# Performance work log

Measured on AMD Instinct MI355X. Metric: run time of the kernel, lower is better.

Reference implementation:

```python
import jax, jax.numpy as jnp
import numpy as np

EMBED_DIM = 1024
NUM_HEADS = 16
HEAD_DIM = EMBED_DIM // NUM_HEADS


def setup_inputs() -> dict:
    key = jax.random.key(0)
    k_x, k_qw, k_qb, k_ow, k_ob = jax.random.split(key, 5)
    B, T, C = 4, 2048, EMBED_DIM
    s = 1.0 / np.sqrt(C)
    return {
        "x": jax.random.normal(k_x, (B, T, C), dtype=jnp.float32),
        # torch nn.Linear weights: [out_features, in_features]
        "qkv_w": jax.random.uniform(k_qw, (3 * C, C), jnp.float32, -s, s),
        "qkv_b": jax.random.uniform(k_qb, (3 * C,), jnp.float32, -s, s),
        "out_w": jax.random.uniform(k_ow, (C, C), jnp.float32, -s, s),
        "out_b": jax.random.uniform(k_ob, (C,), jnp.float32, -s, s),
    }


def reference(x, qkv_w, qkv_b, out_w, out_b):
    B, T, C = x.shape
    H, D = NUM_HEADS, HEAD_DIM
    qkv = x @ qkv_w.T + qkv_b                      # [B,T,3C]
    qkv = qkv.reshape(B, T, 3, H, D).transpose(2, 0, 3, 1, 4)  # [3,B,H,T,D]
    Q, K, V = qkv[0], qkv[1], qkv[2]
    scores = jnp.einsum("bhtd,bhsd->bhts", Q, K) / np.sqrt(D).astype(np.float32)
    causal = jnp.triu(jnp.ones((T, T), dtype=bool), k=1)        # mask future
    scores = jnp.where(causal, -jnp.inf, scores)
    attn_weights = jax.nn.softmax(scores, axis=-1)              # [B,H,T,T]
    out = jnp.einsum("bhts,bhsd->bhtd", attn_weights, V)
    out = out.transpose(0, 2, 1, 3).reshape(B, T, C)
    return out @ out_w.T + out_b, attn_weights
```

## Files before the change

kernel.cpp:

```cpp
#include <hip/hip_runtime.h>
#include <cstdint>
#include <cstddef>

#define Bq  4
#define Tq  2048
#define Cq  1024
#define Hq  16
#define Dq  64
#define BTq 8192
#define C3q 3072

using bf16x8 = __attribute__((ext_vector_type(8))) short;
using f32x4  = __attribute__((ext_vector_type(4))) float;
using us4    = __attribute__((ext_vector_type(4))) unsigned short;

__device__ __forceinline__ unsigned short f2bf(float f) {
  unsigned u = __builtin_bit_cast(unsigned, f);
  return (unsigned short)((u + 0x7fffu + ((u >> 16) & 1u)) >> 16);
}
__device__ __forceinline__ float bf2f(unsigned short h) {
  return __builtin_bit_cast(float, (unsigned)h << 16);
}

__device__ __forceinline__ void gload_lds16(const void* g, void* l) {
  __builtin_amdgcn_global_load_lds(
      (const __attribute__((address_space(1))) void*)g,
      (__attribute__((address_space(3))) void*)l, 16, 0, 0);
}

__global__ __launch_bounds__(256) void cvt_kernel(const float* __restrict__ src,
                                                  unsigned short* __restrict__ dst, int n4) {
  int i = blockIdx.x * 256 + threadIdx.x;
  int stride = gridDim.x * 256;
  for (; i < n4; i += stride) {
    float4 v = reinterpret_cast<const float4*>(src)[i];
    us4 o = { f2bf(v.x), f2bf(v.y), f2bf(v.z), f2bf(v.w) };
    reinterpret_cast<us4*>(dst)[i] = o;
  }
}

template<int EPI>
__global__ __launch_bounds__(256) void gemm128(
    const unsigned short* __restrict__ A, const unsigned short* __restrict__ Bw,
    const float* __restrict__ bias,
    unsigned short* __restrict__ Qb, unsigned short* __restrict__ Kb,
    unsigned short* __restrict__ Vtb, float* __restrict__ Cout,
    int M, int N, int K)
{
  __shared__ unsigned short As[128][32];
  __shared__ unsigned short Bs[128][32];
  const int n0 = blockIdx.x * 128, m0 = blockIdx.y * 128;
  const int tid = threadIdx.x;
  const int w = tid >> 6, l = tid & 63, r = l & 15, g = l >> 4;
  const int wm = w >> 1, wn = w & 1;
  const int ldRow = tid >> 2, ldCol = (tid & 3) * 8;
  f32x4 acc[4][4] = {};

  const unsigned short* Ar0 = A  + (size_t)(m0 +      ldRow) * K + ldCol;
  const unsigned short* Ar1 = A  + (size_t)(m0 + 64 + ldRow) * K + ldCol;
  const unsigned short* Br0 = Bw + (size_t)(n0 +      ldRow) * K + ldCol;
  const unsigned short* Br1 = Bw + (size_t)(n0 + 64 + ldRow) * K + ldCol;
  char* Ab0 = (char*)&As[0][0]        + w * 1024;
  char* Ab1 = (char*)&As[0][0] + 4096 + w * 1024;
  char* Bb0 = (char*)&Bs[0][0]        + w * 1024;
  char* Bb1 = (char*)&Bs[0][0] + 4096 + w * 1024;

  for (int k0 = 0; k0 < K; k0 += 32) {
    __syncthreads();
    gload_lds16(Ar0 + k0, Ab0);
    gload_lds16(Ar1 + k0, Ab1);
    gload_lds16(Br0 + k0, Bb0);
    gload_lds16(Br1 + k0, Bb1);
    __syncthreads();
    bf16x8 a[4], b[4];
    #pragma unroll
    for (int i = 0; i < 4; ++i) a[i] = *(const bf16x8*)&As[wm*64 + i*16 + r][g*8];
    #pragma unroll
    for (int j = 0; j < 4; ++j) b[j] = *(const bf16x8*)&Bs[wn*64 + j*16 + r][g*8];
    #pragma unroll
    for (int i = 0; i < 4; ++i)
      #pragma unroll
      for (int j = 0; j < 4; ++j)
        acc[i][j] = __builtin_amdgcn_mfma_f32_16x16x32_bf16(a[i], b[j], acc[i][j], 0, 0, 0);
  }

  if (EPI == 0) {
    const int which = n0 >> 10;
    #pragma unroll
    for (int i = 0; i < 4; ++i)
      #pragma unroll
      for (int j = 0; j < 4; ++j) {
        int gc  = n0 + wn*64 + j*16 + r;
        int gr0 = m0 + wm*64 + i*16 + 4*g;
        float bv = bias[gc];
        int hd = gc & 1023;
        int h = hd >> 6, d = hd & 63;
        if (which == 2) {
          int b = gr0 >> 11, t0 = gr0 & 2047;
          int bh = b*Hq + h;
          us4 pk = { f2bf(acc[i][j][0] + bv), f2bf(acc[i][j][1] + bv),
                     f2bf(acc[i][j][2] + bv), f2bf(acc[i][j][3] + bv) };
          *(us4*)&Vtb[(size_t)(bh*Dq + d)*Tq + t0] = pk;
        } else {
          unsigned short* dst = which ? Kb : Qb;
          #pragma unroll
          for (int jj = 0; jj < 4; ++jj) {
            int gr = gr0 + jj;
            int b = gr >> 11, t = gr & 2047;
            int bh = b*Hq + h;
            dst[(size_t)(bh*Tq + t)*Dq + d] = f2bf(acc[i][j][jj] + bv);
          }
        }
      }
  } else {
    #pragma unroll
    for (int i = 0; i < 4; ++i)
      #pragma unroll
      for (int j = 0; j < 4; ++j) {
        int gc = n0 + wn*64 + j*16 + r;
        float bv = bias[gc];
        #pragma unroll
        for (int jj = 0; jj < 4; ++jj) {
          int gr = m0 + wm*64 + i*16 + 4*g + jj;
          Cout[(size_t)gr * N + gc] = acc[i][j][jj] + bv;
        }
      }
  }
}

#define PROWB 4224

__global__ __launch_bounds__(256) void attn_kernel(
    const unsigned short* __restrict__ Qb, const unsigned short* __restrict__ Kb,
    const unsigned short* __restrict__ Vtb,
    float* __restrict__ attn, unsigned short* __restrict__ ctxb)
{
  __shared__ __align__(16) unsigned short P[16][2112];
  __shared__ float red[4][32];
  __shared__ float invl_s[32];

  const int p  = blockIdx.x;
  const int bh = blockIdx.y;
  const int tid = threadIdx.x, w = tid >> 6, l = tid & 63, r = l & 15, g = l >> 4;
  const int qbA = p * 16, qbB = (127 - p) * 16;
  const int NA = (qbA + 16 + 31) >> 5;
  const int NB = (qbB + 16 + 31) >> 5;
  const int LAc = NA * 32, LBc = NB * 32;

  const unsigned short* Qp = Qb  + (size_t)bh * Tq * Dq;
  const unsigned short* Kp = Kb  + (size_t)bh * Tq * Dq;
  const unsigned short* Vp = Vtb + (size_t)bh * Dq * Tq;
  char* Pmut = (char*)&P[0][0];

  bf16x8 aqA0 = *(const bf16x8*)&Qp[(size_t)(qbA + r)*Dq      + g*8];
  bf16x8 aqA1 = *(const bf16x8*)&Qp[(size_t)(qbA + r)*Dq + 32 + g*8];
  bf16x8 aqB0 = *(const bf16x8*)&Qp[(size_t)(qbB + r)*Dq      + g*8];
  bf16x8 aqB1 = *(const bf16x8*)&Qp[(size_t)(qbB + r)*Dq + 32 + g*8];

  float lsumA[4] = {0.f,0.f,0.f,0.f}, lsumB[4] = {0.f,0.f,0.f,0.f};

#define CHUNK(k0_, qb_, cb_, q0_, q1_, lsum_)                                       \
  {                                                                                 \
    const int k0c = (k0_);                                                          \
    f32x4 z = {0.f,0.f,0.f,0.f};                                                    \
    bf16x8 bk00 = *(const bf16x8*)&Kp[(size_t)(k0c + r)*Dq      + g*8];             \
    bf16x8 bk01 = *(const bf16x8*)&Kp[(size_t)(k0c + r)*Dq + 32 + g*8];             \
    bf16x8 bk10 = *(const bf16x8*)&Kp[(size_t)(k0c + 16 + r)*Dq      + g*8];        \
    bf16x8 bk11 = *(const bf16x8*)&Kp[(size_t)(k0c + 16 + r)*Dq + 32 + g*8];        \
    __builtin_amdgcn_s_setprio(1);                                                  \
    f32x4 s0 = __builtin_amdgcn_mfma_f32_16x16x32_bf16(q0_, bk00, z, 0, 0, 0);      \
    s0 = __builtin_amdgcn_mfma_f32_16x16x32_bf16(q1_, bk01, s0, 0, 0, 0);           \
    f32x4 s1 = __builtin_amdgcn_mfma_f32_16x16x32_bf16(q0_, bk10, z, 0, 0, 0);      \
    s1 = __builtin_amdgcn_mfma_f32_16x16x32_bf16(q1_, bk11, s1, 0, 0, 0);           \
    __builtin_amdgcn_s_setprio(0);                                                  \
    _Pragma("unroll")                                                               \
    for (int jj = 0; jj < 4; ++jj) {                                                \
      int q = (qb_) + 4*g + jj;                                                     \
      float p0 = (k0c + r      <= q) ? __expf(s0[jj]*0.125f) : 0.f;                 \
      float p1 = (k0c + 16 + r <= q) ? __expf(s1[jj]*0.125f) : 0.f;                 \
      lsum_[jj] += p0 + p1;                                                         \
      int row = 4*g + jj, xm = (row & 7) << 4;                                      \
      *(unsigned short*)(Pmut + row*PROWB + ((((cb_) + r)*2)      ^ xm)) = f2bf(p0);\
      *(unsigned short*)(Pmut + row*PROWB + ((((cb_) + 16 + r)*2) ^ xm)) = f2bf(p1);\
    }                                                                               \
  }

  for (int cj = w; cj < NA; cj += 4)
    CHUNK(cj*32, qbA, cj*32, aqA0, aqA1, lsumA);
  for (int cj = (w - NA) & 3; cj < NB; cj += 4)
    CHUNK(cj*32, qbB, LAc + cj*32, aqB0, aqB1, lsumB);

  #pragma unroll
  for (int jj = 0; jj < 4; ++jj) {
    float sa = lsumA[jj], sb = lsumB[jj];
    #pragma unroll
    for (int off = 1; off < 16; off <<= 1) {
      sa += __shfl_xor(sa, off, 64);
      sb += __shfl_xor(sb, off, 64);
    }
    if (r == 0) { red[w][4*g + jj] = sa; red[w][16 + 4*g + jj] = sb; }
  }
  __syncthreads();
  if (tid < 32) {
    float s = red[0][tid] + red[1][tid] + red[2][tid] + red[3][tid];
    invl_s[tid] = 1.f / s;
  }
  __syncthreads();

  const int row16 = tid >> 4, seg = (tid & 15) * 8;
  const int xm16 = (row16 & 7) << 4;
  const char* Prow = Pmut + row16 * PROWB;
  {
    float inv = invl_s[row16];
    size_t ob = ((size_t)bh*Tq + qbA + row16) * Tq;
    for (int cb = seg; cb < Tq; cb += 128) {
      f32x4 v0 = {0.f,0.f,0.f,0.f}, v1 = {0.f,0.f,0.f,0.f};
      if (cb < LAc) {
        bf16x8 pv = *(const bf16x8*)(Prow + ((cb*2) ^ xm16));
        v0[0]=bf2f((unsigned short)pv[0])*inv; v0[1]=bf2f((unsigned short)pv[1])*inv;
        v0[2]=bf2f((unsigned short)pv[2])*inv; v0[3]=bf2f((unsigned short)pv[3])*inv;
        v1[0]=bf2f((unsigned short)pv[4])*inv; v1[1]=bf2f((unsigned short)pv[5])*inv;
        v1[2]=bf2f((unsigned short)pv[6])*inv; v1[3]=bf2f((unsigned short)pv[7])*inv;
      }
      __builtin_nontemporal_store(v0, (f32x4*)&attn[ob + cb]);
      __builtin_nontemporal_store(v1, (f32x4*)&attn[ob + cb + 4]);
    }
  }
  {
    float inv = invl_s[16 + row16];
    size_t ob = ((size_t)bh*Tq + qbB + row16) * Tq;
    for (int cb = seg; cb < Tq; cb += 128) {
      f32x4 v0 = {0.f,0.f,0.f,0.f}, v1 = {0.f,0.f,0.f,0.f};
      if (cb < LBc) {
        bf16x8 pv = *(const bf16x8*)(Prow + (((LAc + cb)*2) ^ xm16));
        v0[0]=bf2f((unsigned short)pv[0])*inv; v0[1]=bf2f((unsigned short)pv[1])*inv;
        v0[2]=bf2f((unsigned short)pv[2])*inv; v0[3]=bf2f((unsigned short)pv[3])*inv;
        v1[0]=bf2f((unsigned short)pv[4])*inv; v1[1]=bf2f((unsigned short)pv[5])*inv;
        v1[2]=bf2f((unsigned short)pv[6])*inv; v1[3]=bf2f((unsigned short)pv[7])*inv;
      }
      __builtin_nontemporal_store(v0, (f32x4*)&attn[ob + cb]);
      __builtin_nontemporal_store(v1, (f32x4*)&attn[ob + cb + 4]);
    }
  }

  f32x4 coA = {0.f,0.f,0.f,0.f}, coB = {0.f,0.f,0.f,0.f};
  const char* Pr = Pmut + r * PROWB;
  const int xr = (r & 7) << 4;
  const unsigned short* Vrow = &Vp[(size_t)(w*16 + r) * Tq];
  for (int cj = 0; cj < NA; ++cj) {
    int k0 = cj*32;
    bf16x8 pa = *(const bf16x8*)(Pr + (((k0 + g*8)*2) ^ xr));
    bf16x8 bv = *(const bf16x8*)&Vrow[k0 + g*8];
    coA = __builtin_amdgcn_mfma_f32_16x16x32_bf16(pa, bv, coA, 0, 0, 0);
  }
  for (int cj = 0; cj < NB; ++cj) {
    int k0 = cj*32;
    bf16x8 pa = *(const bf16x8*)(Pr + (((LAc + k0 + g*8)*2) ^ xr));
    bf16x8 bv = *(const bf16x8*)&Vrow[k0 + g*8];
    coB = __builtin_amdgcn_mfma_f32_16x16x32_bf16(pa, bv, coB, 0, 0, 0);
  }

  const int b = bh >> 4, h = bh & 15;
  #pragma unroll
  for (int jj = 0; jj < 4; ++jj) {
    int tA = qbA + 4*g + jj;
    ctxb[(size_t)(b*Tq + tA)*Cq + h*Dq + w*16 + r] = f2bf(coA[jj] * invl_s[4*g + jj]);
    int tB = qbB + 4*g + jj;
    ctxb[(size_t)(b*Tq + tB)*Cq + h*Dq + w*16 + r] = f2bf(coB[jj] * invl_s[16 + 4*g + jj]);
  }
#undef CHUNK
}

extern "C" void kernel_launch(void* const* d_in, const int* in_sizes, int n_in,
                              void* d_out, int out_size, void* d_ws, size_t ws_size,
                              hipStream_t stream) {
  const float* x     = (const float*)d_in[0];
  const float* qkv_w = (const float*)d_in[1];
  const float* qkv_b = (const float*)d_in[2];
  const float* out_w = (const float*)d_in[3];
  const float* out_b = (const float*)d_in[4];
  float* out  = (float*)d_out;
  float* attn = out + (size_t)BTq * Cq;

  char* ws = (char*)d_ws;
  unsigned short* xb    = (unsigned short*)(ws);
  unsigned short* wqkvb = (unsigned short*)(ws + (16u << 20));
  unsigned short* woutb = (unsigned short*)(ws + (22u << 20));
  unsigned short* Qb    = (unsigned short*)(ws + (24u << 20));
  unsigned short* Kb    = (unsigned short*)(ws + (40u << 20));
  unsigned short* Vtb   = (unsigned short*)(ws + (56u << 20));
  unsigned short* ctxb  = (unsigned short*)(ws + (72u << 20));

  cvt_kernel<<<2048, 256, 0, stream>>>(x,     xb,    (BTq * Cq) / 4);
  cvt_kernel<<<1024, 256, 0, stream>>>(qkv_w, wqkvb, (C3q * Cq) / 4);
  cvt_kernel<<<512,  256, 0, stream>>>(out_w, woutb, (Cq * Cq) / 4);

  dim3 g1(C3q / 128, BTq / 128);
  gemm128<0><<<g1, 256, 0, stream>>>(xb, wqkvb, qkv_b, Qb, Kb, Vtb, nullptr, BTq, C3q, Cq);

  dim3 g2(64, Bq * Hq);
  attn_kernel<<<g2, 256, 0, stream>>>(Qb, Kb, Vtb, attn, ctxb);

  dim3 g3(Cq / 128, BTq / 128);
  gemm128<1><<<g3, 256, 0, stream>>>(ctxb, woutb, out_b, nullptr, nullptr, nullptr, out, BTq, Cq, Cq);
}
```

Before: 554.5 us.

## Double attention block to 512 threads with prefetched K chunks and split PV reduction

```diff
diff --git a/kernel.cpp b/kernel.cpp
--- a/kernel.cpp
+++ b/kernel.cpp
@@ -129,15 +129,17 @@
 }
 
 #define PROWB 4224
-
-__global__ __launch_bounds__(256) void attn_kernel(
+#define XMASK(row_) ((((row_) & 7) << 4) ^ ((((row_) >> 2) & 3) << 5))
+
+__global__ __launch_bounds__(512, 4) void attn_kernel(
     const unsigned short* __restrict__ Qb, const unsigned short* __restrict__ Kb,
     const unsigned short* __restrict__ Vtb,
     float* __restrict__ attn, unsigned short* __restrict__ ctxb)
 {
   __shared__ __align__(16) unsigned short P[16][2112];
-  __shared__ float red[4][32];
+  __shared__ float red[8][32];
   __shared__ float invl_s[32];
+  __shared__ f32x4 Cred[4][2][64];
 
   const int p  = blockIdx.x;
   const int bh = blockIdx.y;
@@ -159,36 +161,52 @@
 
   float lsumA[4] = {0.f,0.f,0.f,0.f}, lsumB[4] = {0.f,0.f,0.f,0.f};
 
-#define CHUNK(k0_, qb_, cb_, q0_, q1_, lsum_)                                       \
+#define LOADK(ci_, D00, D01, D10, D11)                                              \
   {                                                                                 \
-    const int k0c = (k0_);                                                          \
-    f32x4 z = {0.f,0.f,0.f,0.f};                                                    \
-    bf16x8 bk00 = *(const bf16x8*)&Kp[(size_t)(k0c + r)*Dq      + g*8];             \
-    bf16x8 bk01 = *(const bf16x8*)&Kp[(size_t)(k0c + r)*Dq + 32 + g*8];             \
-    bf16x8 bk10 = *(const bf16x8*)&Kp[(size_t)(k0c + 16 + r)*Dq      + g*8];        \
-    bf16x8 bk11 = *(const bf16x8*)&Kp[(size_t)(k0c + 16 + r)*Dq + 32 + g*8];        \
-    __builtin_amdgcn_s_setprio(1);                                                  \
-    f32x4 s0 = __builtin_amdgcn_mfma_f32_16x16x32_bf16(q0_, bk00, z, 0, 0, 0);      \
-    s0 = __builtin_amdgcn_mfma_f32_16x16x32_bf16(q1_, bk01, s0, 0, 0, 0);           \
-    f32x4 s1 = __builtin_amdgcn_mfma_f32_16x16x32_bf16(q0_, bk10, z, 0, 0, 0);      \
-    s1 = __builtin_amdgcn_mfma_f32_16x16x32_bf16(q1_, bk11, s1, 0, 0, 0);           \
-    __builtin_amdgcn_s_setprio(0);                                                  \
-    _Pragma("unroll")                                                               \
-    for (int jj = 0; jj < 4; ++jj) {                                                \
-      int q = (qb_) + 4*g + jj;                                                     \
-      float p0 = (k0c + r      <= q) ? __expf(s0[jj]*0.125f) : 0.f;                 \
-      float p1 = (k0c + 16 + r <= q) ? __expf(s1[jj]*0.125f) : 0.f;                 \
-      lsum_[jj] += p0 + p1;                                                         \
-      int row = 4*g + jj, xm = (row & 7) << 4;                                      \
-      *(unsigned short*)(Pmut + row*PROWB + ((((cb_) + r)*2)      ^ xm)) = f2bf(p0);\
-      *(unsigned short*)(Pmut + row*PROWB + ((((cb_) + 16 + r)*2) ^ xm)) = f2bf(p1);\
-    }                                                                               \
-  }
-
-  for (int cj = w; cj < NA; cj += 4)
-    CHUNK(cj*32, qbA, cj*32, aqA0, aqA1, lsumA);
-  for (int cj = (w - NA) & 3; cj < NB; cj += 4)
-    CHUNK(cj*32, qbB, LAc + cj*32, aqB0, aqB1, lsumB);
+    int cj_ = ((ci_) < NA) ? (ci_) : (ci_) - NA;                                    \
+    int k0c_ = cj_ * 32;                                                            \
+    D00 = *(const bf16x8*)&Kp[(size_t)(k0c_ + r)*Dq      + g*8];                    \
+    D01 = *(const bf16x8*)&Kp[(size_t)(k0c_ + r)*Dq + 32 + g*8];                    \
+    D10 = *(const bf16x8*)&Kp[(size_t)(k0c_ + 16 + r)*Dq      + g*8];               \
+    D11 = *(const bf16x8*)&Kp[(size_t)(k0c_ + 16 + r)*Dq + 32 + g*8];               \
+  }
+
+  {
+    bf16x8 k00, k01, k10, k11, n00, n01, n10, n11;
+    int ci = w;
+    if (ci < 65) LOADK(ci, k00, k01, k10, k11);
+    for (; ci < 65; ci += 8) {
+      if (ci + 8 < 65) LOADK(ci + 8, n00, n01, n10, n11);
+      const bool isA = ci < NA;
+      const int cj  = isA ? ci : ci - NA;
+      const int k0c = cj * 32;
+      const int qb_ = isA ? qbA : qbB;
+      const int cb_ = isA ? k0c : LAc + k0c;
+      bf16x8 q0_ = isA ? aqA0 : aqB0;
+      bf16x8 q1_ = isA ? aqA1 : aqB1;
+      f32x4 z = {0.f,0.f,0.f,0.f};
+      __builtin_amdgcn_s_setprio(1);
+      f32x4 s0 = __builtin_amdgcn_mfma_f32_16x16x32_bf16(q0_, k00, z, 0, 0, 0);
+      s0 = __builtin_amdgcn_mfma_f32_16x16x32_bf16(q1_, k01, s0, 0, 0, 0);
+      f32x4 s1 = __builtin_amdgcn_mfma_f32_16x16x32_bf16(q0_, k10, z, 0, 0, 0);
+      s1 = __builtin_amdgcn_mfma_f32_16x16x32_bf16(q1_, k11, s1, 0, 0, 0);
+      __builtin_amdgcn_s_setprio(0);
+      float tch[4];
+      #pragma unroll
+      for (int jj = 0; jj < 4; ++jj) {
+        int q = qb_ + 4*g + jj;
+        float p0 = (k0c + r      <= q) ? __expf(s0[jj]*0.125f) : 0.f;
+        float p1 = (k0c + 16 + r <= q) ? __expf(s1[jj]*0.125f) : 0.f;
+        tch[jj] = p0 + p1;
+        int row = 4*g + jj, xm = XMASK(row);
+        *(unsigned short*)(Pmut + row*PROWB + (((cb_ + r)*2)      ^ xm)) = f2bf(p0);
+        *(unsigned short*)(Pmut + row*PROWB + (((cb_ + 16 + r)*2) ^ xm)) = f2bf(p1);
+      }
+      if (isA) { lsumA[0]+=tch[0]; lsumA[1]+=tch[1]; lsumA[2]+=tch[2]; lsumA[3]+=tch[3]; }
+      else     { lsumB[0]+=tch[0]; lsumB[1]+=tch[1]; lsumB[2]+=tch[2]; lsumB[3]+=tch[3]; }
+      k00 = n00; k01 = n01; k10 = n10; k11 = n11;
+    }
+  }
 
   #pragma unroll
   for (int jj = 0; jj < 4; ++jj) {
@@ -202,21 +220,27 @@
   }
   __syncthreads();
   if (tid < 32) {
-    float s = red[0][tid] + red[1][tid] + red[2][tid] + red[3][tid];
+    float s = 0.f;
+    #pragma unroll
+    for (int ww = 0; ww < 8; ++ww) s += red[ww][tid];
     invl_s[tid] = 1.f / s;
   }
   __syncthreads();
 
-  const int row16 = tid >> 4, seg = (tid & 15) * 8;
-  const int xm16 = (row16 & 7) << 4;
-  const char* Prow = Pmut + row16 * PROWB;
   {
-    float inv = invl_s[row16];
-    size_t ob = ((size_t)bh*Tq + qbA + row16) * Tq;
+    const int s16   = tid >> 8;
+    const int row16 = (tid >> 4) & 15;
+    const int seg   = (tid & 15) * 8;
+    const int xm16  = XMASK(row16);
+    const char* Prow = Pmut + row16 * PROWB;
+    const int Lc    = s16 ? LBc : LAc;
+    const int cbase = s16 ? LAc : 0;
+    float inv = invl_s[s16*16 + row16];
+    size_t ob = ((size_t)bh*Tq + (s16 ? qbB : qbA) + row16) * Tq;
     for (int cb = seg; cb < Tq; cb += 128) {
       f32x4 v0 = {0.f,0.f,0.f,0.f}, v1 = {0.f,0.f,0.f,0.f};
-      if (cb < LAc) {
-        bf16x8 pv = *(const bf16x8*)(Prow + ((cb*2) ^ xm16));
+      if (cb < Lc) {
+        bf16x8 pv = *(const bf16x8*)(Prow + (((cbase + cb)*2) ^ xm16));
         v0[0]=bf2f((unsigned short)pv[0])*inv; v0[1]=bf2f((unsigned short)pv[1])*inv;
         v0[2]=bf2f((unsigned short)pv[2])*inv; v0[3]=bf2f((unsigned short)pv[3])*inv;
         v1[0]=bf2f((unsigned short)pv[4])*inv; v1[1]=bf2f((unsigned short)pv[5])*inv;
@@ -226,49 +250,51 @@
       __builtin_nontemporal_store(v1, (f32x4*)&attn[ob + cb + 4]);
     }
   }
+
+  f32x4 coA = {0.f,0.f,0.f,0.f}, coB = {0.f,0.f,0.f,0.f};
   {
-    float inv = invl_s[16 + row16];
-    size_t ob = ((size_t)bh*Tq + qbB + row16) * Tq;
-    for (int cb = seg; cb < Tq; cb += 128) {
-      f32x4 v0 = {0.f,0.f,0.f,0.f}, v1 = {0.f,0.f,0.f,0.f};
-      if (cb < LBc) {
-        bf16x8 pv = *(const bf16x8*)(Prow + (((LAc + cb)*2) ^ xm16));
-        v0[0]=bf2f((unsigned short)pv[0])*inv; v0[1]=bf2f((unsigned short)pv[1])*inv;
-        v0[2]=bf2f((unsigned short)pv[2])*inv; v0[3]=bf2f((unsigned short)pv[3])*inv;
-        v1[0]=bf2f((unsigned short)pv[4])*inv; v1[1]=bf2f((unsigned short)pv[5])*inv;
-        v1[2]=bf2f((unsigned short)pv[6])*inv; v1[3]=bf2f((unsigned short)pv[7])*inv;
-      }
-      __builtin_nontemporal_store(v0, (f32x4*)&attn[ob + cb]);
-      __builtin_nontemporal_store(v1, (f32x4*)&attn[ob + cb + 4]);
-    }
-  }
-
-  f32x4 coA = {0.f,0.f,0.f,0.f}, coB = {0.f,0.f,0.f,0.f};
-  const char* Pr = Pmut + r * PROWB;
-  const int xr = (r & 7) << 4;
-  const unsigned short* Vrow = &Vp[(size_t)(w*16 + r) * Tq];
-  for (int cj = 0; cj < NA; ++cj) {
-    int k0 = cj*32;
-    bf16x8 pa = *(const bf16x8*)(Pr + (((k0 + g*8)*2) ^ xr));
-    bf16x8 bv = *(const bf16x8*)&Vrow[k0 + g*8];
-    coA = __builtin_amdgcn_mfma_f32_16x16x32_bf16(pa, bv, coA, 0, 0, 0);
-  }
-  for (int cj = 0; cj < NB; ++cj) {
-    int k0 = cj*32;
-    bf16x8 pa = *(const bf16x8*)(Pr + (((LAc + k0 + g*8)*2) ^ xr));
-    bf16x8 bv = *(const bf16x8*)&Vrow[k0 + g*8];
-    coB = __builtin_amdgcn_mfma_f32_16x16x32_bf16(pa, bv, coB, 0, 0, 0);
-  }
-
-  const int b = bh >> 4, h = bh & 15;
-  #pragma unroll
-  for (int jj = 0; jj < 4; ++jj) {
-    int tA = qbA + 4*g + jj;
-    ctxb[(size_t)(b*Tq + tA)*Cq + h*Dq + w*16 + r] = f2bf(coA[jj] * invl_s[4*g + jj]);
-    int tB = qbB + 4*g + jj;
-    ctxb[(size_t)(b*Tq + tB)*Cq + h*Dq + w*16 + r] = f2bf(coB[jj] * invl_s[16 + 4*g + jj]);
-  }
-#undef CHUNK
+    const int dblk = w & 3, par = w >> 2;
+    const char* Pr = Pmut + r * PROWB;
+    const int xr = XMASK(r);
+    const unsigned short* Vrow = &Vp[(size_t)(dblk*16 + r) * Tq];
+    bf16x8 pa, bv, pan, bvn;
+    int ci = par;
+    {
+      int cj = (ci < NA) ? ci : ci - NA;
+      int cb = (ci < NA) ? ci*32 : LAc + cj*32;
+      pa = *(const bf16x8*)(Pr + (((cb + g*8)*2) ^ xr));
+      bv = *(const bf16x8*)&Vrow[cj*32 + g*8];
+    }
+    for (; ci < 65; ci += 2) {
+      if (ci + 2 < 65) {
+        int cn = ci + 2;
+        int cj = (cn < NA) ? cn : cn - NA;
+        int cb = (cn < NA) ? cn*32 : LAc + cj*32;
+        pan = *(const bf16x8*)(Pr + (((cb + g*8)*2) ^ xr));
+        bvn = *(const bf16x8*)&Vrow[cj*32 + g*8];
+      }
+      if (ci < NA) coA = __builtin_amdgcn_mfma_f32_16x16x32_bf16(pa, bv, coA, 0, 0, 0);
+      else         coB = __builtin_amdgcn_mfma_f32_16x16x32_bf16(pa, bv, coB, 0, 0, 0);
+      pa = pan; bv = bvn;
+    }
+    if (par == 1) { Cred[dblk][0][l] = coA; Cred[dblk][1][l] = coB; }
+  }
+  __syncthreads();
+  if ((w >> 2) == 0) {
+    const int dblk = w & 3;
+    f32x4 cA = Cred[dblk][0][l], cB = Cred[dblk][1][l];
+    coA[0]+=cA[0]; coA[1]+=cA[1]; coA[2]+=cA[2]; coA[3]+=cA[3];
+    coB[0]+=cB[0]; coB[1]+=cB[1]; coB[2]+=cB[2]; coB[3]+=cB[3];
+    const int b = bh >> 4, h = bh & 15;
+    #pragma unroll
+    for (int jj = 0; jj < 4; ++jj) {
+      int tA = qbA + 4*g + jj;
+      ctxb[(size_t)(b*Tq + tA)*Cq + h*Dq + dblk*16 + r] = f2bf(coA[jj] * invl_s[4*g + jj]);
+      int tB = qbB + 4*g + jj;
+      ctxb[(size_t)(b*Tq + tB)*Cq + h*Dq + dblk*16 + r] = f2bf(coB[jj] * invl_s[16 + 4*g + jj]);
+    }
+  }
+#undef LOADK
 }
 
 extern "C" void kernel_launch(void* const* d_in, const int* in_sizes, int n_in,
@@ -299,7 +325,7 @@
   gemm128<0><<<g1, 256, 0, stream>>>(xb, wqkvb, qkv_b, Qb, Kb, Vtb, nullptr, BTq, C3q, Cq);
 
   dim3 g2(64, Bq * Hq);
-  attn_kernel<<<g2, 256, 0, stream>>>(Qb, Kb, Vtb, attn, ctxb);
+  attn_kernel<<<g2, 512, 0, stream>>>(Qb, Kb, Vtb, attn, ctxb);
 
   dim3 g3(Cq / 128, BTq / 128);
   gemm128<1><<<g3, 256, 0, stream>>>(ctxb, woutb, out_b, nullptr, nullptr, nullptr, out, BTq, Cq, Cq);
```

After: 511.3 us. 1.08x faster.
